# Kernel tuning notes

Hardware: AMD Instinct MI355X
Metric: run time of the kernel (lower is better)

The kernel has to match this reference:

```python
import jax, jax.numpy as jnp
import numpy as np

TEMPERATURE = 0.5  # init temperature; attn_drop=0.0 so dropout is identity


def setup_inputs() -> dict:
    key = jax.random.key(0)
    k1, k2, k3 = jax.random.split(key, 3)
    B, H, N, D = 4, 8, 2048, 64
    q = jax.random.normal(k1, (B, H, N, D), dtype=jnp.float32)
    k = jax.random.normal(k2, (B, H, N, D), dtype=jnp.float32)
    v = jax.random.normal(k3, (B, H, N, D), dtype=jnp.float32)
    scale = jnp.asarray(D ** -0.5, dtype=jnp.float32)
    return {"q": q, "k": k, "v": v, "scale": scale}


def reference(q, k, v, scale):
    # logits: [B,H,N,N]
    logits = jnp.einsum("bhqd,bhkd->bhqk", q, k) * scale
    # first softmax acts as a soft mask over keys
    soft_mask = jax.nn.softmax(logits / TEMPERATURE, axis=-1)
    # second softmax over masked logits (elementwise product, NOT matmul)
    attn = jax.nn.softmax(logits * soft_mask, axis=-1)
    # dropout with p=0.0 is identity
    out = jnp.einsum("bhqk,bhkd->bhqd", attn, v)
    return out
```

## Files before the change

kernel.cpp:

```cpp
#include <hip/hip_runtime.h>


typedef _Float16 f16;
typedef f16 f16x8 __attribute__((ext_vector_type(8)));
typedef float f32x4 __attribute__((ext_vector_type(4)));

#define MFMA(a, b, c) __builtin_amdgcn_mfma_f32_16x16x32_f16((a), (b), (c), 0, 0, 0)
#define EXP2(x) __builtin_amdgcn_exp2f(x)

#define N_CTX 2048
#define DH 64
#define KT 64
#define NKT (N_CTX / KT)
#define ROWS 128
#define QS 72

#define C2 2.885390081777927f

__device__ inline unsigned pk(float a, float b) {
    typedef __fp16 fp16x2_t __attribute__((ext_vector_type(2)));
    union { fp16x2_t v; unsigned u; } x;
    x.v = __builtin_amdgcn_cvt_pkrtz(a, b);
    return x.u;
}

__global__ __launch_bounds__(512, 4)
void stk_attn_mfma(const float* __restrict__ qg, const float* __restrict__ kg,
                   const float* __restrict__ vglob, const float* __restrict__ sg,
                   float* __restrict__ og) {
    __shared__ f16 Qs[ROWS * QS];
    __shared__ f16 Ks[2][KT * QS];
    __shared__ f16 Vt[2][DH * QS];
    __shared__ f16 Ps[8][16 * QS];

    const int tid  = threadIdx.x;
    const int wv   = tid >> 6;
    const int lane = tid & 63;
    const int l15  = lane & 15;
    const int q4   = lane >> 4;
    const int vp   = tid & 31;
    const int vgr  = tid >> 5;
    const int bh   = blockIdx.x & 31;
    const int q0   = (blockIdx.x >> 5) * ROWS;
    const float scale2 = sg[0] * C2;

    const float* qb = qg + (size_t)bh * N_CTX * DH;
    const float* kb = kg + (size_t)bh * N_CTX * DH;
    const float* vb = vglob + (size_t)bh * N_CTX * DH;
    float*       ob = og + (size_t)bh * N_CTX * DH;

    #pragma unroll
    for (int it = 0; it < 4; ++it) {
        int idx = it * 512 + tid;
        int row = idx >> 4, c4 = idx & 15;
        float4 v = *(const float4*)&qb[((size_t)(q0 + row)) * DH + c4 * 4];
        *(uint2*)&Qs[row * QS + c4 * 4] =
            make_uint2(pk(v.x * scale2, v.y * scale2), pk(v.z * scale2, v.w * scale2));
    }
    __syncthreads();

    f16x8 aq[2];
    #pragma unroll
    for (int kc = 0; kc < 2; ++kc)
        aq[kc] = *(const f16x8*)&Qs[(wv * 16 + l15) * QS + kc * 32 + q4 * 8];

    f16* const ks_w  = &Ks[0][0];
    const f16* const ks_r = &Ks[0][l15 * QS + q4 * 8];
    f16* const vt_w  = &Vt[0][(vgr * 4) * QS + 2 * vp];
    const f16* const vt_r = &Vt[0][l15 * QS + q4 * 8];
    f16* const ps_w  = &Ps[wv][(q4 * 4) * QS + l15];
    const f16* const ps_r = &Ps[wv][l15 * QS + q4 * 8];
    const int KSB = KT * QS;

    float s1[4] = {0, 0, 0, 0};
    float4 kr[2];
    #pragma unroll
    for (int it = 0; it < 2; ++it) {
        int idx = it * 512 + tid;
        kr[it] = *(const float4*)&kb[((size_t)(idx >> 4)) * DH + (idx & 15) * 4];
    }
    #pragma unroll
    for (int it = 0; it < 2; ++it) {
        int idx = it * 512 + tid;
        *(uint2*)&ks_w[(idx >> 4) * QS + (idx & 15) * 4] =
            make_uint2(pk(kr[it].x, kr[it].y), pk(kr[it].z, kr[it].w));
    }
    #pragma unroll
    for (int it = 0; it < 2; ++it) {
        int idx = it * 512 + tid;
        kr[it] = *(const float4*)&kb[((size_t)KT + (idx >> 4)) * DH + (idx & 15) * 4];
    }
    __syncthreads();

    for (int kt = 0; kt < NKT; ++kt) {
        const int cur = (kt & 1) * KSB, nxt = KSB - cur;
        #pragma unroll
        for (int it = 0; it < 2; ++it) {
            int idx = it * 512 + tid;
            *(uint2*)&ks_w[nxt + (idx >> 4) * QS + (idx & 15) * 4] =
                make_uint2(pk(kr[it].x, kr[it].y), pk(kr[it].z, kr[it].w));
        }
        {
            int tn = (kt + 2 < NKT) ? kt + 2 : NKT - 1;
            #pragma unroll
            for (int it = 0; it < 2; ++it) {
                int idx = it * 512 + tid;
                kr[it] = *(const float4*)&kb[((size_t)tn * KT + (idx >> 4)) * DH + (idx & 15) * 4];
            }
        }
        #pragma unroll
        for (int kgi = 0; kgi < 4; ++kgi) {
            f16x8 b0 = *(const f16x8*)&ks_r[cur + kgi * 16 * QS];
            f16x8 b1 = *(const f16x8*)&ks_r[cur + kgi * 16 * QS + 32];
            f32x4 acc = {0.f, 0.f, 0.f, 0.f};
            acc = MFMA(aq[0], b0, acc);
            acc = MFMA(aq[1], b1, acc);
            #pragma unroll
            for (int r = 0; r < 4; ++r)
                s1[r] += EXP2(acc[r]);
        }
        __syncthreads();
    }
    float inv1[4];
    #pragma unroll
    for (int s = 0; s < 4; ++s) {
        float v = s1[s];
        v += __shfl_xor(v, 1, 64);
        v += __shfl_xor(v, 2, 64);
        v += __shfl_xor(v, 4, 64);
        v += __shfl_xor(v, 8, 64);
        inv1[s] = 0.5f / v;
    }

    float l2[4] = {0, 0, 0, 0};
    f32x4 O[4];
    #pragma unroll
    for (int dt = 0; dt < 4; ++dt) O[dt] = (f32x4){0.f, 0.f, 0.f, 0.f};

    float4 vr[2];
    #pragma unroll
    for (int it = 0; it < 2; ++it) {
        int idx = it * 512 + tid;
        kr[it] = *(const float4*)&kb[((size_t)(idx >> 4)) * DH + (idx & 15) * 4];
    }
    #pragma unroll
    for (int it = 0; it < 2; ++it) {
        int idx = it * 512 + tid;
        *(uint2*)&ks_w[(idx >> 4) * QS + (idx & 15) * 4] =
            make_uint2(pk(kr[it].x, kr[it].y), pk(kr[it].z, kr[it].w));
    }
    {
        const float* vs = vb + ((size_t)2 * vp) * DH + vgr * 4;
        vr[0] = *(const float4*)(vs);
        vr[1] = *(const float4*)(vs + DH);
        #pragma unroll
        for (int j = 0; j < 4; ++j)
            *(unsigned*)&vt_w[j * QS] =
                pk(((const float*)&vr[0])[j], ((const float*)&vr[1])[j]);
        const float* vs1 = vb + ((size_t)KT + 2 * vp) * DH + vgr * 4;
        vr[0] = *(const float4*)(vs1);
        vr[1] = *(const float4*)(vs1 + DH);
    }
    #pragma unroll
    for (int it = 0; it < 2; ++it) {
        int idx = it * 512 + tid;
        kr[it] = *(const float4*)&kb[((size_t)KT + (idx >> 4)) * DH + (idx & 15) * 4];
    }
    __syncthreads();

    for (int kt = 0; kt < NKT; ++kt) {
        const int cur = (kt & 1) * KSB, nxt = KSB - cur;
        #pragma unroll
        for (int it = 0; it < 2; ++it) {
            int idx = it * 512 + tid;
            *(uint2*)&ks_w[nxt + (idx >> 4) * QS + (idx & 15) * 4] =
                make_uint2(pk(kr[it].x, kr[it].y), pk(kr[it].z, kr[it].w));
        }
        #pragma unroll
        for (int j = 0; j < 4; ++j)
            *(unsigned*)&vt_w[nxt + j * QS] =
                pk(((const float*)&vr[0])[j], ((const float*)&vr[1])[j]);
        #pragma unroll
        for (int kgi = 0; kgi < 4; ++kgi) {
            f16x8 b0 = *(const f16x8*)&ks_r[cur + kgi * 16 * QS];
            f16x8 b1 = *(const f16x8*)&ks_r[cur + kgi * 16 * QS + 32];
            f32x4 acc = {0.f, 0.f, 0.f, 0.f};
            acc = MFMA(aq[0], b0, acc);
            acc = MFMA(aq[1], b1, acc);
            #pragma unroll
            for (int r = 0; r < 4; ++r) {
                float a  = acc[r];
                float e1 = EXP2(a);
                float e2 = EXP2((a * e1) * inv1[r]);
                l2[r] += e2;
                ps_w[r * QS + kgi * 16] = (f16)e2;
            }
        }
        {
            int tn = (kt + 2 < NKT) ? kt + 2 : NKT - 1;
            #pragma unroll
            for (int it = 0; it < 2; ++it) {
                int idx = it * 512 + tid;
                kr[it] = *(const float4*)&kb[((size_t)tn * KT + (idx >> 4)) * DH + (idx & 15) * 4];
            }
            const float* vs = vb + ((size_t)tn * KT + 2 * vp) * DH + vgr * 4;
            vr[0] = *(const float4*)(vs);
            vr[1] = *(const float4*)(vs + DH);
        }
        #pragma unroll
        for (int kc = 0; kc < 2; ++kc) {
            f16x8 ap = *(const f16x8*)&ps_r[kc * 32];
            #pragma unroll
            for (int dt = 0; dt < 4; ++dt) {
                f16x8 bv = *(const f16x8*)&vt_r[cur + dt * 16 * QS + kc * 32];
                O[dt] = MFMA(ap, bv, O[dt]);
            }
        }
        __syncthreads();
    }

    float invl2[4];
    #pragma unroll
    for (int s = 0; s < 4; ++s) {
        float v = l2[s];
        v += __shfl_xor(v, 1, 64);
        v += __shfl_xor(v, 2, 64);
        v += __shfl_xor(v, 4, 64);
        v += __shfl_xor(v, 8, 64);
        invl2[s] = 1.0f / v;
    }
    #pragma unroll
    for (int dt = 0; dt < 4; ++dt)
        #pragma unroll
        for (int r = 0; r < 4; ++r) {
            int row = q0 + wv * 16 + q4 * 4 + r;
            ob[(size_t)row * DH + dt * 16 + l15] = O[dt][r] * invl2[r];
        }
}

extern "C" void kernel_launch(void* const* d_in, const int* in_sizes, int n_in,
                              void* d_out, int out_size, void* d_ws, size_t ws_size,
                              hipStream_t stream) {
    const float* q = (const float*)d_in[0];
    const float* k = (const float*)d_in[1];
    const float* v = (const float*)d_in[2];
    const float* s = (const float*)d_in[3];
    float* out = (float*)d_out;
    dim3 grid(32 * 16);
    stk_attn_mfma<<<grid, 512, 0, stream>>>(q, k, v, s, out);
}
```

Baseline: 169.5 us.

## Transpose QK MFMA so P stays in registers, drop Q/P shared staging

```diff
diff --git a/kernel.cpp b/kernel.cpp
--- a/kernel.cpp
+++ b/kernel.cpp
@@ -3,9 +3,11 @@
 
 typedef _Float16 f16;
 typedef f16 f16x8 __attribute__((ext_vector_type(8)));
+typedef f16 f16x4 __attribute__((ext_vector_type(4)));
 typedef float f32x4 __attribute__((ext_vector_type(4)));
 
-#define MFMA(a, b, c) __builtin_amdgcn_mfma_f32_16x16x32_f16((a), (b), (c), 0, 0, 0)
+#define MFMA32(a, b, c) __builtin_amdgcn_mfma_f32_16x16x32_f16((a), (b), (c), 0, 0, 0)
+#define MFMA16(a, b, c) __builtin_amdgcn_mfma_f32_16x16x16f16((a), (b), (c), 0, 0, 0)
 #define EXP2(x) __builtin_amdgcn_exp2f(x)
 
 #define N_CTX 2048
@@ -28,10 +30,8 @@
 void stk_attn_mfma(const float* __restrict__ qg, const float* __restrict__ kg,
                    const float* __restrict__ vglob, const float* __restrict__ sg,
                    float* __restrict__ og) {
-    __shared__ f16 Qs[ROWS * QS];
     __shared__ f16 Ks[2][KT * QS];
     __shared__ f16 Vt[2][DH * QS];
-    __shared__ f16 Ps[8][16 * QS];
 
     const int tid  = threadIdx.x;
     const int wv   = tid >> 6;
@@ -49,30 +49,29 @@
     const float* vb = vglob + (size_t)bh * N_CTX * DH;
     float*       ob = og + (size_t)bh * N_CTX * DH;
 
-    #pragma unroll
-    for (int it = 0; it < 4; ++it) {
-        int idx = it * 512 + tid;
-        int row = idx >> 4, c4 = idx & 15;
-        float4 v = *(const float4*)&qb[((size_t)(q0 + row)) * DH + c4 * 4];
-        *(uint2*)&Qs[row * QS + c4 * 4] =
-            make_uint2(pk(v.x * scale2, v.y * scale2), pk(v.z * scale2, v.w * scale2));
-    }
-    __syncthreads();
-
     f16x8 aq[2];
-    #pragma unroll
-    for (int kc = 0; kc < 2; ++kc)
-        aq[kc] = *(const f16x8*)&Qs[(wv * 16 + l15) * QS + kc * 32 + q4 * 8];
+    {
+        const float* qrow = qb + (size_t)(q0 + wv * 16 + l15) * DH;
+        #pragma unroll
+        for (int kc = 0; kc < 2; ++kc) {
+            float4 a0 = *(const float4*)&qrow[kc * 32 + q4 * 8];
+            float4 a1 = *(const float4*)&qrow[kc * 32 + q4 * 8 + 4];
+            union { f16x8 h; unsigned u[4]; } A;
+            A.u[0] = pk(a0.x * scale2, a0.y * scale2);
+            A.u[1] = pk(a0.z * scale2, a0.w * scale2);
+            A.u[2] = pk(a1.x * scale2, a1.y * scale2);
+            A.u[3] = pk(a1.z * scale2, a1.w * scale2);
+            aq[kc] = A.h;
+        }
+    }
 
     f16* const ks_w  = &Ks[0][0];
     const f16* const ks_r = &Ks[0][l15 * QS + q4 * 8];
     f16* const vt_w  = &Vt[0][(vgr * 4) * QS + 2 * vp];
-    const f16* const vt_r = &Vt[0][l15 * QS + q4 * 8];
-    f16* const ps_w  = &Ps[wv][(q4 * 4) * QS + l15];
-    const f16* const ps_r = &Ps[wv][l15 * QS + q4 * 8];
+    const f16* const vt_r = &Vt[0][l15 * QS + q4 * 4];
     const int KSB = KT * QS;
 
-    float s1[4] = {0, 0, 0, 0};
+    float s1 = 0.f;
     float4 kr[2];
     #pragma unroll
     for (int it = 0; it < 2; ++it) {
@@ -113,26 +112,20 @@
             f16x8 b0 = *(const f16x8*)&ks_r[cur + kgi * 16 * QS];
             f16x8 b1 = *(const f16x8*)&ks_r[cur + kgi * 16 * QS + 32];
             f32x4 acc = {0.f, 0.f, 0.f, 0.f};
-            acc = MFMA(aq[0], b0, acc);
-            acc = MFMA(aq[1], b1, acc);
-            #pragma unroll
-            for (int r = 0; r < 4; ++r)
-                s1[r] += EXP2(acc[r]);
+            acc = MFMA32(b0, aq[0], acc);
+            acc = MFMA32(b1, aq[1], acc);
+            s1 += EXP2(acc[0]);
+            s1 += EXP2(acc[1]);
+            s1 += EXP2(acc[2]);
+            s1 += EXP2(acc[3]);
         }
         __syncthreads();
     }
-    float inv1[4];
-    #pragma unroll
-    for (int s = 0; s < 4; ++s) {
-        float v = s1[s];
-        v += __shfl_xor(v, 1, 64);
-        v += __shfl_xor(v, 2, 64);
-        v += __shfl_xor(v, 4, 64);
-        v += __shfl_xor(v, 8, 64);
-        inv1[s] = 0.5f / v;
-    }
-
-    float l2[4] = {0, 0, 0, 0};
+    s1 += __shfl_xor(s1, 16, 64);
+    s1 += __shfl_xor(s1, 32, 64);
+    const float inv1 = 0.5f / s1;
+
+    float l2 = 0.f;
     f32x4 O[4];
     #pragma unroll
     for (int dt = 0; dt < 4; ++dt) O[dt] = (f32x4){0.f, 0.f, 0.f, 0.f};
@@ -180,21 +173,27 @@
         for (int j = 0; j < 4; ++j)
             *(unsigned*)&vt_w[nxt + j * QS] =
                 pk(((const float*)&vr[0])[j], ((const float*)&vr[1])[j]);
+        f16x4 pfr[4];
         #pragma unroll
         for (int kgi = 0; kgi < 4; ++kgi) {
             f16x8 b0 = *(const f16x8*)&ks_r[cur + kgi * 16 * QS];
             f16x8 b1 = *(const f16x8*)&ks_r[cur + kgi * 16 * QS + 32];
             f32x4 acc = {0.f, 0.f, 0.f, 0.f};
-            acc = MFMA(aq[0], b0, acc);
-            acc = MFMA(aq[1], b1, acc);
+            acc = MFMA32(b0, aq[0], acc);
+            acc = MFMA32(b1, aq[1], acc);
+            float e2r[4];
             #pragma unroll
             for (int r = 0; r < 4; ++r) {
                 float a  = acc[r];
                 float e1 = EXP2(a);
-                float e2 = EXP2((a * e1) * inv1[r]);
-                l2[r] += e2;
-                ps_w[r * QS + kgi * 16] = (f16)e2;
-            }
+                float e2 = EXP2((a * e1) * inv1);
+                l2 += e2;
+                e2r[r] = e2;
+            }
+            union { f16x4 h; unsigned u[2]; } P;
+            P.u[0] = pk(e2r[0], e2r[1]);
+            P.u[1] = pk(e2r[2], e2r[3]);
+            pfr[kgi] = P.h;
         }
         {
             int tn = (kt + 2 < NKT) ? kt + 2 : NKT - 1;
@@ -208,34 +207,29 @@
             vr[1] = *(const float4*)(vs + DH);
         }
         #pragma unroll
-        for (int kc = 0; kc < 2; ++kc) {
-            f16x8 ap = *(const f16x8*)&ps_r[kc * 32];
+        for (int kgi = 0; kgi < 4; ++kgi) {
             #pragma unroll
             for (int dt = 0; dt < 4; ++dt) {
-                f16x8 bv = *(const f16x8*)&vt_r[cur + dt * 16 * QS + kc * 32];
-                O[dt] = MFMA(ap, bv, O[dt]);
+                f16x4 av = *(const f16x4*)&vt_r[cur + dt * 16 * QS + kgi * 16];
+                O[dt] = MFMA16(av, pfr[kgi], O[dt]);
             }
         }
         __syncthreads();
     }
 
-    float invl2[4];
-    #pragma unroll
-    for (int s = 0; s < 4; ++s) {
-        float v = l2[s];
-        v += __shfl_xor(v, 1, 64);
-        v += __shfl_xor(v, 2, 64);
-        v += __shfl_xor(v, 4, 64);
-        v += __shfl_xor(v, 8, 64);
-        invl2[s] = 1.0f / v;
-    }
-    #pragma unroll
-    for (int dt = 0; dt < 4; ++dt)
-        #pragma unroll
-        for (int r = 0; r < 4; ++r) {
-            int row = q0 + wv * 16 + q4 * 4 + r;
-            ob[(size_t)row * DH + dt * 16 + l15] = O[dt][r] * invl2[r];
-        }
+    l2 += __shfl_xor(l2, 16, 64);
+    l2 += __shfl_xor(l2, 32, 64);
+    const float invl2 = 1.0f / l2;
+    const size_t orow = (size_t)(q0 + wv * 16 + l15) * DH;
+    #pragma unroll
+    for (int dt = 0; dt < 4; ++dt) {
+        float4 o;
+        o.x = O[dt][0] * invl2;
+        o.y = O[dt][1] * invl2;
+        o.z = O[dt][2] * invl2;
+        o.w = O[dt][3] * invl2;
+        *(float4*)&ob[orow + dt * 16 + q4 * 4] = o;
+    }
 }
 
 extern "C" void kernel_launch(void* const* d_in, const int* in_sizes, int n_in,
```

After: 167.7 us. Within noise of the previous version (-1.1%).
